# Kernel optimization log

Measured on AMD Instinct MI355X. Metric: run time of the kernel, lower is better.

The kernel has to match this reference:

```python
import jax, jax.numpy as jnp
import numpy as np
from jax import lax

BOX_STRIDES = (32, 64, 128, 256)
MASK_STRIDE = 4
MASK_SIZE = 28
PATCH = 512
TOPK = 64
SCORE_TH = 0.5
IOU_TH = 0.5
MASK_TH = 0.5


def setup_inputs():
    key = jax.random.key(0)
    ks = jax.random.split(key, 10)
    d = {}
    d["pred0"] = jax.random.normal(ks[0], (2, 6, 16, 16), jnp.float32)
    d["pred1"] = jax.random.normal(ks[1], (2, 6, 8, 8), jnp.float32)
    d["pred2"] = jax.random.normal(ks[2], (2, 6, 4, 4), jnp.float32)
    d["pred3"] = jax.random.normal(ks[3], (2, 6, 2, 2), jnp.float32)
    d["feat0"] = jax.random.normal(ks[4], (2, 64, 128, 128), jnp.float32)
    d["feat1"] = jax.random.normal(ks[5], (2, 64, 64, 64), jnp.float32)
    d["feat2"] = jax.random.normal(ks[6], (2, 64, 32, 32), jnp.float32)
    d["feat3"] = jax.random.normal(ks[7], (2, 64, 16, 16), jnp.float32)
    d["w1"] = jax.random.normal(ks[8], (128, 256, 3, 3), jnp.float32) * 0.05
    d["b1"] = jnp.zeros((128,), jnp.float32)
    d["w2"] = jax.random.normal(ks[9], (1, 128, 1, 1), jnp.float32) * 0.05
    d["b2"] = jnp.zeros((1,), jnp.float32)
    return d


def _decode_level(pred, stride):
    # pred: [B, 6, H, W] -> [B, H*W, 6], (cx,cy)=(p+grid)*stride, wh=exp(p)*stride
    B, no, H, W = pred.shape
    p = pred.transpose(0, 2, 3, 1).reshape(B, H * W, no)
    gy, gx = jnp.meshgrid(jnp.arange(H), jnp.arange(W), indexing="ij")
    grid = jnp.stack([gx.ravel(), gy.ravel()], axis=-1).astype(p.dtype)  # [HW,2] (x,y)
    xy = (p[..., 0:2] + grid) * stride
    wh = jnp.exp(p[..., 2:4]) * stride
    return jnp.concatenate([xy, wh, p[..., 4:]], axis=-1)


def _iou_matrix(b):
    # b: [K,4] xyxy
    area = jnp.clip(b[:, 2] - b[:, 0], 0) * jnp.clip(b[:, 3] - b[:, 1], 0)
    ix0 = jnp.maximum(b[:, None, 0], b[None, :, 0])
    iy0 = jnp.maximum(b[:, None, 1], b[None, :, 1])
    ix1 = jnp.minimum(b[:, None, 2], b[None, :, 2])
    iy1 = jnp.minimum(b[:, None, 3], b[None, :, 3])
    inter = jnp.clip(ix1 - ix0, 0) * jnp.clip(iy1 - iy0, 0)
    union = area[:, None] + area[None, :] - inter
    return inter / jnp.maximum(union, 1e-9)


def _nms_keep(boxes, labels, valid):
    # boxes already sorted by descending score; batched NMS via per-class coord offset
    off = labels.astype(boxes.dtype)[:, None] * (PATCH * 8.0)
    iou = _iou_matrix(boxes + off)
    idx = jnp.arange(TOPK)

    def body(i, keep):
        sup = keep[i] & (iou[i] > IOU_TH) & (idx > i)
        return keep & ~sup

    return lax.fori_loop(0, TOPK, body, valid)


def _roi_align_one(feat, box):
    # feat: [C,Hf,Wf]; box: [4] xyxy in image coords (spatial_scale=1/MASK_STRIDE)
    # torchvision-style aligned=False, one bilinear sample per bin center
    C, Hf, Wf = feat.shape
    b = box / MASK_STRIDE
    bw = (b[2] - b[0]) / MASK_SIZE
    bh = (b[3] - b[1]) / MASK_SIZE
    xs = b[0] + (jnp.arange(MASK_SIZE, dtype=feat.dtype) + 0.5) * bw
    ys = b[1] + (jnp.arange(MASK_SIZE, dtype=feat.dtype) + 0.5) * bh
    x = jnp.clip(jnp.broadcast_to(xs[None, :], (MASK_SIZE, MASK_SIZE)), 0.0, Wf - 1.0)
    y = jnp.clip(jnp.broadcast_to(ys[:, None], (MASK_SIZE, MASK_SIZE)), 0.0, Hf - 1.0)
    x0 = jnp.floor(x).astype(jnp.int32)
    y0 = jnp.floor(y).astype(jnp.int32)
    x1 = jnp.minimum(x0 + 1, Wf - 1)
    y1 = jnp.minimum(y0 + 1, Hf - 1)
    fx = x - x0
    fy = y - y0
    v00 = feat[:, y0, x0]
    v01 = feat[:, y0, x1]
    v10 = feat[:, y1, x0]
    v11 = feat[:, y1, x1]
    return (v00 * (1 - fy) * (1 - fx) + v01 * (1 - fy) * fx
            + v10 * fy * (1 - fx) + v11 * fy * fx)  # [C,S,S]


def _paste_one(mask_soft, box_int):
    # nearest-neighbor upsample of [S,S] mask into its box on a [P,P] canvas
    x0, y0, x1, y1 = box_int[0], box_int[1], box_int[2], box_int[3]
    h = y1 - y0 + 1
    w = x1 - x0 + 1
    ys = jnp.arange(PATCH, dtype=jnp.int32)
    xs = jnp.arange(PATCH, dtype=jnp.int32)
    iy = jnp.clip((ys - y0) * MASK_SIZE // h, 0, MASK_SIZE - 1)
    ix = jnp.clip((xs - x0) * MASK_SIZE // w, 0, MASK_SIZE - 1)
    g = mask_soft[iy][:, ix]  # [P,P]
    inside = ((ys >= y0) & (ys <= y1))[:, None] & ((xs >= x0) & (xs <= x1))[None, :]
    return jnp.where(inside, g, 0.0)


def _conv(x, w, b, pad):
    y = lax.conv_general_dilated(x, w, (1, 1), pad, dimension_numbers=("NCHW", "OIHW", "NCHW"))
    return y + b[None, :, None, None]


def _pipeline(pred0, pred1, pred2, pred3, feat0, feat1, feat2, feat3, w1, b1, w2, b2):
    # box branch: decode per-level predictions
    yolo = jnp.concatenate(
        [_decode_level(p, s) for p, s in zip([pred0, pred1, pred2, pred3], BOX_STRIDES)],
        axis=1,
    )  # [B,N,6]
    B = yolo.shape[0]
    cx, cy, w_, h_ = yolo[..., 0], yolo[..., 1], yolo[..., 2], yolo[..., 3]
    boxes = jnp.stack([cx - w_ / 2, cy - h_ / 2, cx + w_ / 2, cy + h_ / 2], axis=-1)
    scores = jax.nn.sigmoid(yolo[..., 4])
    labels = jnp.argmax(yolo[..., 5:], axis=-1)
    valid = scores > SCORE_TH
    top_scores, top_idx = lax.top_k(jnp.where(valid, scores, 0.0), TOPK)
    boxes_k = jnp.take_along_axis(boxes, top_idx[..., None], axis=1)  # [B,K,4]
    labels_k = jnp.take_along_axis(labels, top_idx, axis=1)
    valid_k = top_scores > SCORE_TH
    keep = jax.vmap(_nms_keep)(boxes_k, labels_k, valid_k)  # [B,K] bool

    # mask branch: merge mask feats at the first level's resolution (nearest)
    H0, W0 = feat0.shape[2], feat0.shape[3]
    merged = jnp.concatenate(
        [feat0] + [jax.image.resize(f, (B, f.shape[1], H0, W0), "nearest") for f in [feat1, feat2, feat3]],
        axis=1,
    )  # [B,256,H0,W0]
    rois = jax.vmap(lambda f, bx: jax.vmap(lambda bb: _roi_align_one(f, bb))(bx))(merged, boxes_k)
    C = rois.shape[2]
    x = rois.reshape(B * TOPK, C, MASK_SIZE, MASK_SIZE)
    hdn = jax.nn.silu(_conv(x, w1, b1, "SAME"))
    logits = _conv(hdn, w2, b2, "SAME")  # [B*K,1,S,S]
    soft = jax.nn.sigmoid(logits).reshape(B, TOPK, MASK_SIZE, MASK_SIZE)

    box_int = jnp.clip(boxes_k, 0, PATCH - 1).astype(jnp.int32)
    pasted = jax.vmap(jax.vmap(_paste_one))(soft, box_int)  # [B,K,P,P]
    return top_scores, boxes_k, labels_k, pasted, keep


def reference(pred0, pred1, pred2, pred3, feat0, feat1, feat2, feat3, w1, b1, w2, b2):
    top_scores, boxes_k, labels_k, pasted, keep = _pipeline(
        pred0, pred1, pred2, pred3, feat0, feat1, feat2, feat3, w1, b1, w2, b2
    )
    out_scores = top_scores * keep
    bin_masks = (pasted > MASK_TH) & keep[:, :, None, None]
    return out_scores, boxes_k, labels_k.astype(jnp.int32), bin_masks, keep
```

## Files before the change

### kernel.cpp

```cpp
#include <hip/hip_runtime.h>
#include <hip/hip_bf16.h>
#include <cstdint>

#define NTOPK 64
#define A_TOT 340
#define MS 28

#define OFF_SCORES 0
#define OFF_BOXES  128
#define OFF_LABELS 640
#define OFF_MASKS  768
#define OFF_KEEP   33555200ull

typedef __attribute__((ext_vector_type(4))) float f32x4;
typedef __attribute__((ext_vector_type(2))) float f32x2;
typedef long fp8x8;

__device__ __forceinline__ float sigmoidf_(float x) { return 1.f / (1.f + expf(-x)); }
__device__ __forceinline__ float bf2f(unsigned u) {
  return __uint_as_float(u << 16);
}
__device__ __forceinline__ unsigned short f2bf(float f) {
  __hip_bfloat16 h = __float2bfloat16(f);
  return *(unsigned short*)&h;
}

__global__ __launch_bounds__(256) void k_prep(
    const float* __restrict__ p0, const float* __restrict__ p1,
    const float* __restrict__ p2, const float* __restrict__ p3,
    const float* __restrict__ f0, const float* __restrict__ f1,
    const float* __restrict__ f2, const float* __restrict__ f3,
    const float* __restrict__ w1,
    float* __restrict__ out,
    float* __restrict__ ws_boxes, int* __restrict__ ws_keep,
    int* __restrict__ ws_boxint,
    unsigned char* __restrict__ wt, unsigned short* __restrict__ mg)
{
  __shared__ __align__(16) char smem_raw[128 * 260 * 2];
  const int bid = blockIdx.x;
  const int t = threadIdx.x;

  if (bid < 2) {
    const int b = bid;
    float* sc = (float*)smem_raw;
    float(*bx)[4] = (float(*)[4])(sc + A_TOT);
    float* tk_score = (float*)(bx + A_TOT);
    float(*tk_box)[4] = (float(*)[4])(tk_score + 64);

    for (int a = t; a < A_TOT; a += 256) {
      const float* pp; int W, HW, la; float stride;
      if (a < 256)      { pp = p0; W = 16; HW = 256; la = a;       stride = 32.f;  }
      else if (a < 320) { pp = p1; W = 8;  HW = 64;  la = a - 256; stride = 64.f;  }
      else if (a < 336) { pp = p2; W = 4;  HW = 16;  la = a - 320; stride = 128.f; }
      else              { pp = p3; W = 2;  HW = 4;   la = a - 336; stride = 256.f; }
      const float* base = pp + (size_t)b * 6 * HW + la;
      float v0 = base[0], v1 = base[HW], v2 = base[2 * HW], v3 = base[3 * HW], v4 = base[4 * HW];
      int gx = la % W, gy = la / W;
      float cx = (v0 + (float)gx) * stride;
      float cy = (v1 + (float)gy) * stride;
      float w_ = expf(v2) * stride;
      float h_ = expf(v3) * stride;
      float score = sigmoidf_(v4);
      sc[a] = (score > 0.5f) ? score : 0.f;
      bx[a][0] = cx - 0.5f * w_;
      bx[a][1] = cy - 0.5f * h_;
      bx[a][2] = cx + 0.5f * w_;
      bx[a][3] = cy + 0.5f * h_;
    }
    __syncthreads();

    for (int a = t; a < A_TOT; a += 256) {
      float my = sc[a];
      int rank = 0;
      for (int j = 0; j < A_TOT; ++j) {
        float o = sc[j];
        rank += (o > my) || (o == my && j < a);
      }
      if (rank < NTOPK) {
        tk_score[rank] = my;
        tk_box[rank][0] = bx[a][0];
        tk_box[rank][1] = bx[a][1];
        tk_box[rank][2] = bx[a][2];
        tk_box[rank][3] = bx[a][3];
      }
    }
    __syncthreads();

    if (t < NTOPK) {
      float x0 = tk_box[t][0], y0 = tk_box[t][1];
      float x1 = tk_box[t][2], y1 = tk_box[t][3];
      float s = tk_score[t];
      float area = fmaxf(x1 - x0, 0.f) * fmaxf(y1 - y0, 0.f);
      int keep = (s > 0.5f) ? 1 : 0;
      for (int i = 0; i < NTOPK - 1; ++i) {
        int   ki = __shfl(keep, i);
        float a0 = __shfl(x0, i);
        float c0 = __shfl(y0, i);
        float a1 = __shfl(x1, i);
        float c1 = __shfl(y1, i);
        float ai = __shfl(area, i);
        if (ki && t > i && keep) {
          float ix0 = fmaxf(a0, x0), iy0 = fmaxf(c0, y0);
          float ix1 = fminf(a1, x1), iy1 = fminf(c1, y1);
          float inter = fmaxf(ix1 - ix0, 0.f) * fmaxf(iy1 - iy0, 0.f);
          float uni = ai + area - inter;
          float iou = inter / fmaxf(uni, 1e-9f);
          if (iou > 0.5f) keep = 0;
        }
      }
      int box = b * NTOPK + t;
      out[OFF_SCORES + box] = keep ? s : 0.f;
      float bv[4] = {x0, y0, x1, y1};
      #pragma unroll
      for (int c = 0; c < 4; ++c) {
        out[OFF_BOXES + box * 4 + c] = bv[c];
        ws_boxes[box * 4 + c] = bv[c];
        float bc = fminf(fmaxf(bv[c], 0.f), 511.f);
        ws_boxint[box * 4 + c] = (int)bc;
      }
      out[OFF_LABELS + box] = 0.f;
      out[OFF_KEEP + box] = keep ? 1.f : 0.f;
      ws_keep[box] = keep;
    }
    return;
  }

  if (bid < 130) {
    const int co = bid - 2;
    const int ci = t;
    const int c = ci >> 5, cil = ci & 31;
    const int cq = co >> 5, col = co & 31;
    const int slot = ((cil >> 3) ^ ((col >> 2) & 3)) * 8 + (cil & 7);
    const float* src = w1 + ((size_t)co * 256 + ci) * 9;
    #pragma unroll
    for (int tap = 0; tap < 9; ++tap) {
      unsigned u = __builtin_amdgcn_cvt_pk_fp8_f32(src[tap], 0.f, 0, false);
      wt[(((size_t)(c * 4 + cq) * 9 + tap)) * 1024 + col * 32 + slot] =
          (unsigned char)(u & 0xff);
    }
    return;
  }

  {
    const int idx = bid - 130;
    const int b = idx >> 7;
    const int y = idx & 127;
    unsigned short* tile = (unsigned short*)smem_raw;
    const int x = t & 127, ch = t >> 7;

    {
      const float* src = f0 + ((size_t)b * 64) * 16384 + y * 128 + x;
      for (int cc = 0; cc < 32; ++cc) {
        int cl = ch * 32 + cc;
        tile[x * 260 + cl] = f2bf(src[(size_t)cl * 16384]);
      }
    }
    {
      const float* src = f1 + ((size_t)b * 64) * 4096 + (y >> 1) * 64 + (x >> 1);
      for (int cc = 0; cc < 32; ++cc) {
        int cl = ch * 32 + cc;
        tile[x * 260 + 64 + cl] = f2bf(src[(size_t)cl * 4096]);
      }
    }
    {
      const float* src = f2 + ((size_t)b * 64) * 1024 + (y >> 2) * 32 + (x >> 2);
      for (int cc = 0; cc < 32; ++cc) {
        int cl = ch * 32 + cc;
        tile[x * 260 + 128 + cl] = f2bf(src[(size_t)cl * 1024]);
      }
    }
    {
      const float* src = f3 + ((size_t)b * 64) * 256 + (y >> 3) * 16 + (x >> 3);
      for (int cc = 0; cc < 32; ++cc) {
        int cl = ch * 32 + cc;
        tile[x * 260 + 192 + cl] = f2bf(src[(size_t)cl * 256]);
      }
    }
    __syncthreads();
    unsigned short* dst = mg + (((size_t)b * 128 + y) * 128) * 256;
    for (int it = 0; it < 32; ++it) {
      int qq = t + it * 256;
      int xx = qq >> 6, cg = qq & 63;
      *(ushort4*)(dst + xx * 256 + cg * 4) = *(ushort4*)&tile[xx * 260 + cg * 4];
    }
  }
}

__global__ __launch_bounds__(512, 4) void k_conv(
    const unsigned short* __restrict__ mg,
    const unsigned char* __restrict__ wt,
    const float* __restrict__ b1, const float* __restrict__ w2,
    const float* __restrict__ b2,
    const float* __restrict__ ws_boxes, const int* __restrict__ ws_keep,
    const int* __restrict__ ws_boxint,
    float* __restrict__ out)
{
  const int bid = blockIdx.x;
  const int boxLo = bid & 7;
  const int r1 = bid >> 3;
  const int q = r1 & 3;
  const int box = ((r1 >> 2) << 3) | boxLo;
  const int t = threadIdx.x;

  float* mb = out + OFF_MASKS + (size_t)box * 262144;

  if (!ws_keep[box]) {
    f32x4 z = {0.f, 0.f, 0.f, 0.f};
    f32x4* p = (f32x4*)(mb + (size_t)q * 128 * 512);
    for (int e = t; e < 16384; e += 512)
      __builtin_nontemporal_store(z, p + e);
    return;
  }

  const int lane = t & 63, wv = t >> 6;
  const int cq = wv >> 1, half = wv & 1;
  const int laneN = lane & 15, kg = lane >> 4;

  __shared__ __align__(16) unsigned char lds[46080];
  __shared__ float psum[4][200];
  __shared__ float softm[7][28];
  __shared__ int   xa_s[MS], xb_s[MS];
  __shared__ float fx_s[MS];
  __shared__ int   ya_s[9], yb_s[9];
  __shared__ float fy_s[9];
  __shared__ float byf[4];
  __shared__ int   bii[4];

  if (t < 4) { byf[t] = ws_boxes[box * 4 + t]; bii[t] = ws_boxint[box * 4 + t]; }
  __syncthreads();
  {
    const float b0 = byf[0] * 0.25f, b1_ = byf[1] * 0.25f;
    const float b2_ = byf[2] * 0.25f, b3_ = byf[3] * 0.25f;
    if (t < MS) {
      float bw = (b2_ - b0) * (1.f / MS);
      float x = b0 + ((float)t + 0.5f) * bw;
      x = fminf(fmaxf(x, 0.f), 127.f);
      int x0 = (int)floorf(x);
      xa_s[t] = x0; xb_s[t] = min(x0 + 1, 127); fx_s[t] = x - (float)x0;
    }
    if (t < 9) {
      int gr = q * 7 + t - 1;
      if (gr < 0 || gr > 27) {
        ya_s[t] = -1; yb_s[t] = 0; fy_s[t] = 0.f;
      } else {
        float bh = (b3_ - b1_) * (1.f / MS);
        float yy = b1_ + ((float)gr + 0.5f) * bh;
        yy = fminf(fmaxf(yy, 0.f), 127.f);
        int ya = (int)floorf(yy);
        ya_s[t] = ya; yb_s[t] = min(ya + 1, 127); fy_s[t] = yy - (float)ya;
      }
    }
  }

  int badd[7][3];
  bool act[7];
  #pragma unroll
  for (int i = 0; i < 7; ++i) {
    int tile = half * 7 + i;
    act[i] = tile < 13;
    int p = tile * 16 + laneN;
    if (p > 195) p = 195;
    int py = p / 28, px = p - py * 28;
    #pragma unroll
    for (int dx = 0; dx < 3; ++dx) {
      int cell = px + dx;
      badd[i][dx] = 36864 + py * 1024 + cell * 32 + (kg ^ ((cell >> 2) & 3)) * 8;
    }
  }
  const int aswz = (kg ^ ((laneN >> 2) & 3)) * 8;

  f32x4 acc[2][7];
  #pragma unroll
  for (int m = 0; m < 2; ++m)
    #pragma unroll
    for (int i = 0; i < 7; ++i) acc[m][i] = (f32x4){0.f, 0.f, 0.f, 0.f};

  const uint4* wbase = (const uint4*)wt;
  const unsigned short* mgb = mg + ((size_t)(box >> 6) * 128 * 128) * 256;

  uint4 ga0, ga1, ga2, ga3, ga4;
  auto issueA = [&](int c) {
    const uint4* wa = wbase + (size_t)c * 2304;
    ga0 = wa[t]; ga1 = wa[t + 512]; ga2 = wa[t + 1024]; ga3 = wa[t + 1536];
    if (t < 256) ga4 = wa[t + 2048];
  };
  auto writeA = [&]() {
    uint4* da = (uint4*)lds;
    da[t] = ga0; da[t + 512] = ga1; da[t + 1024] = ga2; da[t + 1536] = ga3;
    if (t < 256) da[t + 2048] = ga4;
  };

  issueA(0);
  const unsigned char* la = lds + (size_t)cq * 9216;
  __syncthreads();

  #pragma unroll 1
  for (int c = 0; c < 8; ++c) {
    writeA();
    #pragma unroll 1
    for (int e = t; e < 1152; e += 512) {
      int r = e >> 7, rem = e & 127;
      int cell = rem >> 2, quad = rem & 3;
      unsigned char* dst = lds + 36864 + r * 1024 + cell * 32 +
                           (quad ^ ((cell >> 2) & 3)) * 8;
      int gc = cell - 1;
      int ya = ya_s[r];
      if (gc < 0 || gc > 27 || ya < 0) {
        uint2 z = {0u, 0u};
        *(uint2*)dst = z;
        continue;
      }
      int yb = yb_s[r];
      float fy = fy_s[r];
      int U = c * 4 + quad;
      int xa = xa_s[gc], xb = xb_s[gc];
      float fx = fx_s[gc];
      float w00 = (1.f - fy) * (1.f - fx), w01 = (1.f - fy) * fx;
      float w10 = fy * (1.f - fx),         w11 = fy * fx;
      uint4 A = *(const uint4*)(mgb + ((size_t)(ya * 128 + xa)) * 256 + U * 8);
      uint4 B = *(const uint4*)(mgb + ((size_t)(ya * 128 + xb)) * 256 + U * 8);
      uint4 C = *(const uint4*)(mgb + ((size_t)(yb * 128 + xa)) * 256 + U * 8);
      uint4 D = *(const uint4*)(mgb + ((size_t)(yb * 128 + xb)) * 256 + U * 8);
      const unsigned* pa = (const unsigned*)&A;
      const unsigned* pb = (const unsigned*)&B;
      const unsigned* pc = (const unsigned*)&C;
      const unsigned* pd = (const unsigned*)&D;
      float f[8];
      #pragma unroll
      for (int k2 = 0; k2 < 4; ++k2) {
        f[2 * k2] = bf2f(pa[k2] & 0xffffu) * w00 + bf2f(pb[k2] & 0xffffu) * w01 +
                    bf2f(pc[k2] & 0xffffu) * w10 + bf2f(pd[k2] & 0xffffu) * w11;
        f[2 * k2 + 1] = bf2f(pa[k2] >> 16) * w00 + bf2f(pb[k2] >> 16) * w01 +
                        bf2f(pc[k2] >> 16) * w10 + bf2f(pd[k2] >> 16) * w11;
      }
      unsigned o0 = __builtin_amdgcn_cvt_pk_fp8_f32(f[0], f[1], 0, false);
      o0 = __builtin_amdgcn_cvt_pk_fp8_f32(f[2], f[3], o0, true);
      unsigned o1 = __builtin_amdgcn_cvt_pk_fp8_f32(f[4], f[5], 0, false);
      o1 = __builtin_amdgcn_cvt_pk_fp8_f32(f[6], f[7], o1, true);
      uint2 pk; pk.x = o0; pk.y = o1;
      *(uint2*)dst = pk;
    }
    __syncthreads();
    if (c < 7) issueA(c + 1);
    #pragma unroll
    for (int tap = 0; tap < 9; ++tap) {
      const int dy = tap / 3, dx = tap - dy * 3;
      fp8x8 av0 = *(const fp8x8*)(la + tap * 1024 + laneN * 32 + aswz);
      fp8x8 av1 = *(const fp8x8*)(la + tap * 1024 + 512 + laneN * 32 + aswz);
      #pragma unroll
      for (int i = 0; i < 7; ++i) {
        if (act[i]) {
          fp8x8 bv = *(const fp8x8*)(lds + badd[i][dx] + dy * 1024);
          acc[0][i] = __builtin_amdgcn_mfma_f32_16x16x32_fp8_fp8(av0, bv, acc[0][i], 0, 0, 0);
          acc[1][i] = __builtin_amdgcn_mfma_f32_16x16x32_fp8_fp8(av1, bv, acc[1][i], 0, 0, 0);
        }
      }
    }
    __syncthreads();
  }

  {
    float b1v[2][4], w2v[2][4];
    #pragma unroll
    for (int m = 0; m < 2; ++m)
      #pragma unroll
      for (int r = 0; r < 4; ++r) {
        int co = cq * 32 + m * 16 + kg * 4 + r;
        b1v[m][r] = b1[co];
        w2v[m][r] = w2[co];
      }
    #pragma unroll
    for (int i = 0; i < 7; ++i) {
      if (!act[i]) continue;
      float part = 0.f;
      #pragma unroll
      for (int m = 0; m < 2; ++m)
        #pragma unroll
        for (int r = 0; r < 4; ++r) {
          float h = acc[m][i][r] + b1v[m][r];
          part = fmaf(w2v[m][r], h * sigmoidf_(h), part);
        }
      part += __shfl_xor(part, 16);
      part += __shfl_xor(part, 32);
      int p = (half * 7 + i) * 16 + laneN;
      if (kg == 0 && p < 196)
        psum[cq][p] = part;
    }
  }
  __syncthreads();

  if (t < 196) {
    float s = sigmoidf_(psum[0][t] + psum[1][t] + psum[2][t] + psum[3][t] + b2[0]);
    softm[t / 28][t % 28] = s;
  }
  __syncthreads();

  {
    const int x0 = bii[0], y0 = bii[1], x1 = bii[2], y1 = bii[3];
    const int w = x1 - x0 + 1, h = y1 - y0 + 1;
    int Ylo = (q == 0) ? 0 : (y0 + (q * 7 * h + 27) / 28);
    int Yhi = (q == 3) ? 512 : (y0 + ((q + 1) * 7 * h + 27) / 28);
    Ylo = min(max(Ylo, 0), 512);
    Yhi = min(max(Yhi, Ylo), 512);

    const int c4 = (t & 255) * 2;
    const int rr = t >> 8;
    int ixr[2];
    bool inx[2];
    #pragma unroll
    for (int u = 0; u < 2; ++u) {
      int X = c4 + u;
      int vx = (X - x0) * MS;
      int ix = (vx >= 0) ? (vx / w) : 0;
      ixr[u] = min(max(ix, 0), MS - 1);
      inx[u] = (X >= x0) && (X <= x1);
    }

    #pragma unroll 1
    for (int Y = Ylo + rr; Y < Yhi; Y += 2) {
      f32x2 o = {0.f, 0.f};
      if (Y >= y0 && Y <= y1) {
        int vy = (Y - y0) * MS;
        int iy = min(vy / h, MS - 1);
        const float* srow = &softm[iy - q * 7][0];
        o.x = (inx[0] && srow[ixr[0]] > 0.5f) ? 1.f : 0.f;
        o.y = (inx[1] && srow[ixr[1]] > 0.5f) ? 1.f : 0.f;
      }
      __builtin_nontemporal_store(o, (f32x2*)(mb + (size_t)Y * 512 + c4));
    }
  }
}

extern "C" void kernel_launch(void* const* d_in, const int* in_sizes, int n_in,
                              void* d_out, int out_size, void* d_ws, size_t ws_size,
                              hipStream_t stream) {
  const float* p0 = (const float*)d_in[0];
  const float* p1 = (const float*)d_in[1];
  const float* p2 = (const float*)d_in[2];
  const float* p3 = (const float*)d_in[3];
  const float* f0 = (const float*)d_in[4];
  const float* f1 = (const float*)d_in[5];
  const float* f2 = (const float*)d_in[6];
  const float* f3 = (const float*)d_in[7];
  const float* w1 = (const float*)d_in[8];
  const float* b1 = (const float*)d_in[9];
  const float* w2 = (const float*)d_in[10];
  const float* b2 = (const float*)d_in[11];
  float* out = (float*)d_out;

  float* wsf = (float*)d_ws;
  float*          ws_boxes  = wsf;
  int*            ws_keep   = (int*)(wsf + 512);
  int*            ws_boxint = (int*)(wsf + 640);
  unsigned char*  ws_wt     = (unsigned char*)(wsf + 402560);
  unsigned short* ws_merged = (unsigned short*)(wsf + 476288);

  k_prep<<<386, 256, 0, stream>>>(p0, p1, p2, p3, f0, f1, f2, f3, w1,
                                  out, ws_boxes, ws_keep, ws_boxint,
                                  ws_wt, ws_merged);
  k_conv<<<512, 512, 0, stream>>>(ws_merged, ws_wt, b1, w2, b2,
                                  ws_boxes, ws_keep, ws_boxint, out);
}
```

Before: 256.2 us.

## Software-pipeline ROI gather with MFMA and vectorize mask paste stores

The bilinear ROI gather for the next channel chunk now starts its global loads (weights and the first feature element) before the current chunk's MFMA taps, so memory latency overlaps compute. The fp8 conversion and LDS write run after the compute barrier, with an extra barrier per iteration. The mask paste now writes 16-byte float4 stores, four rows per pass, and restricts the box-row loop to rows inside the box. Rows outside the box are zero-filled in a separate loop spread across the four quarter-blocks. This adds register pressure and an extra sync per chunk.

```diff
diff --git a/kernel.cpp b/kernel.cpp
--- a/kernel.cpp
+++ b/kernel.cpp
@@ -13,7 +13,6 @@
 #define OFF_KEEP   33555200ull
 
 typedef __attribute__((ext_vector_type(4))) float f32x4;
-typedef __attribute__((ext_vector_type(2))) float f32x2;
 typedef long fp8x8;
 
 __device__ __forceinline__ float sigmoidf_(float x) { return 1.f / (1.f + expf(-x)); }
@@ -290,58 +289,75 @@
     if (t < 256) da[t + 2048] = ga4;
   };
 
+  auto loadI = [&](int i, int cn, uint4& A, uint4& B, uint4& C, uint4& D) -> bool {
+    int e = t + i * 512;
+    int r = e >> 7, rem = e & 127;
+    int cell = rem >> 2, quad = rem & 3;
+    int gc = cell - 1;
+    int ya = ya_s[r];
+    if (gc < 0 || gc > 27 || ya < 0) return true;
+    int yb = yb_s[r];
+    int xa = xa_s[gc], xb = xb_s[gc];
+    const unsigned short* bU = mgb + (size_t)(cn * 4 + quad) * 8;
+    A = *(const uint4*)(bU + (size_t)(ya * 128 + xa) * 256);
+    B = *(const uint4*)(bU + (size_t)(ya * 128 + xb) * 256);
+    C = *(const uint4*)(bU + (size_t)(yb * 128 + xa) * 256);
+    D = *(const uint4*)(bU + (size_t)(yb * 128 + xb) * 256);
+    return false;
+  };
+  auto cvtW = [&](int i, bool sk, uint4 A, uint4 B, uint4 C, uint4 D) {
+    int e = t + i * 512;
+    int r = e >> 7, rem = e & 127;
+    int cell = rem >> 2, quad = rem & 3;
+    int gc = cell - 1;
+    unsigned char* dst = lds + 36864 + r * 1024 + cell * 32 +
+                         ((quad ^ ((cell >> 2) & 3)) << 3);
+    if (sk) { uint2 z = {0u, 0u}; *(uint2*)dst = z; return; }
+    float fy = fy_s[r], fx = fx_s[gc];
+    float w00 = (1.f - fy) * (1.f - fx), w01 = (1.f - fy) * fx;
+    float w10 = fy * (1.f - fx),         w11 = fy * fx;
+    const unsigned* pa = (const unsigned*)&A;
+    const unsigned* pb = (const unsigned*)&B;
+    const unsigned* pc = (const unsigned*)&C;
+    const unsigned* pd = (const unsigned*)&D;
+    float f[8];
+    #pragma unroll
+    for (int k2 = 0; k2 < 4; ++k2) {
+      f[2 * k2] = bf2f(pa[k2] & 0xffffu) * w00 + bf2f(pb[k2] & 0xffffu) * w01 +
+                  bf2f(pc[k2] & 0xffffu) * w10 + bf2f(pd[k2] & 0xffffu) * w11;
+      f[2 * k2 + 1] = bf2f(pa[k2] >> 16) * w00 + bf2f(pb[k2] >> 16) * w01 +
+                      bf2f(pc[k2] >> 16) * w10 + bf2f(pd[k2] >> 16) * w11;
+    }
+    unsigned o0 = __builtin_amdgcn_cvt_pk_fp8_f32(f[0], f[1], 0, false);
+    o0 = __builtin_amdgcn_cvt_pk_fp8_f32(f[2], f[3], o0, true);
+    unsigned o1 = __builtin_amdgcn_cvt_pk_fp8_f32(f[4], f[5], 0, false);
+    o1 = __builtin_amdgcn_cvt_pk_fp8_f32(f[6], f[7], o1, true);
+    uint2 pk; pk.x = o0; pk.y = o1;
+    *(uint2*)dst = pk;
+  };
+
   issueA(0);
+  writeA();
+  {
+    uint4 A, B, C, D;
+    bool s0 = loadI(0, 0, A, B, C, D); cvtW(0, s0, A, B, C, D);
+    bool s1 = loadI(1, 0, A, B, C, D); cvtW(1, s1, A, B, C, D);
+    if (t < 128) {
+      bool s2 = loadI(2, 0, A, B, C, D); cvtW(2, s2, A, B, C, D);
+    }
+  }
   const unsigned char* la = lds + (size_t)cq * 9216;
   __syncthreads();
 
   #pragma unroll 1
   for (int c = 0; c < 8; ++c) {
-    writeA();
-    #pragma unroll 1
-    for (int e = t; e < 1152; e += 512) {
-      int r = e >> 7, rem = e & 127;
-      int cell = rem >> 2, quad = rem & 3;
-      unsigned char* dst = lds + 36864 + r * 1024 + cell * 32 +
-                           (quad ^ ((cell >> 2) & 3)) * 8;
-      int gc = cell - 1;
-      int ya = ya_s[r];
-      if (gc < 0 || gc > 27 || ya < 0) {
-        uint2 z = {0u, 0u};
-        *(uint2*)dst = z;
-        continue;
-      }
-      int yb = yb_s[r];
-      float fy = fy_s[r];
-      int U = c * 4 + quad;
-      int xa = xa_s[gc], xb = xb_s[gc];
-      float fx = fx_s[gc];
-      float w00 = (1.f - fy) * (1.f - fx), w01 = (1.f - fy) * fx;
-      float w10 = fy * (1.f - fx),         w11 = fy * fx;
-      uint4 A = *(const uint4*)(mgb + ((size_t)(ya * 128 + xa)) * 256 + U * 8);
-      uint4 B = *(const uint4*)(mgb + ((size_t)(ya * 128 + xb)) * 256 + U * 8);
-      uint4 C = *(const uint4*)(mgb + ((size_t)(yb * 128 + xa)) * 256 + U * 8);
-      uint4 D = *(const uint4*)(mgb + ((size_t)(yb * 128 + xb)) * 256 + U * 8);
-      const unsigned* pa = (const unsigned*)&A;
-      const unsigned* pb = (const unsigned*)&B;
-      const unsigned* pc = (const unsigned*)&C;
-      const unsigned* pd = (const unsigned*)&D;
-      float f[8];
-      #pragma unroll
-      for (int k2 = 0; k2 < 4; ++k2) {
-        f[2 * k2] = bf2f(pa[k2] & 0xffffu) * w00 + bf2f(pb[k2] & 0xffffu) * w01 +
-                    bf2f(pc[k2] & 0xffffu) * w10 + bf2f(pd[k2] & 0xffffu) * w11;
-        f[2 * k2 + 1] = bf2f(pa[k2] >> 16) * w00 + bf2f(pb[k2] >> 16) * w01 +
-                        bf2f(pc[k2] >> 16) * w10 + bf2f(pd[k2] >> 16) * w11;
-      }
-      unsigned o0 = __builtin_amdgcn_cvt_pk_fp8_f32(f[0], f[1], 0, false);
-      o0 = __builtin_amdgcn_cvt_pk_fp8_f32(f[2], f[3], o0, true);
-      unsigned o1 = __builtin_amdgcn_cvt_pk_fp8_f32(f[4], f[5], 0, false);
-      o1 = __builtin_amdgcn_cvt_pk_fp8_f32(f[6], f[7], o1, true);
-      uint2 pk; pk.x = o0; pk.y = o1;
-      *(uint2*)dst = pk;
-    }
-    __syncthreads();
-    if (c < 7) issueA(c + 1);
+    const bool pf = (c < 7);
+    uint4 A0, B0, C0, D0;
+    bool s0 = true;
+    if (pf) {
+      issueA(c + 1);
+      s0 = loadI(0, c + 1, A0, B0, C0, D0);
+    }
     #pragma unroll
     for (int tap = 0; tap < 9; ++tap) {
       const int dy = tap / 3, dx = tap - dy * 3;
@@ -357,6 +373,21 @@
       }
     }
     __syncthreads();
+    if (pf) {
+      writeA();
+      cvtW(0, s0, A0, B0, C0, D0);
+      {
+        uint4 A1, B1, C1, D1;
+        bool s1 = loadI(1, c + 1, A1, B1, C1, D1);
+        cvtW(1, s1, A1, B1, C1, D1);
+      }
+      if (t < 128) {
+        uint4 A2, B2, C2, D2;
+        bool s2 = loadI(2, c + 1, A2, B2, C2, D2);
+        cvtW(2, s2, A2, B2, C2, D2);
+      }
+      __syncthreads();
+    }
   }
 
   {
@@ -398,35 +429,41 @@
   {
     const int x0 = bii[0], y0 = bii[1], x1 = bii[2], y1 = bii[3];
     const int w = x1 - x0 + 1, h = y1 - y0 + 1;
-    int Ylo = (q == 0) ? 0 : (y0 + (q * 7 * h + 27) / 28);
-    int Yhi = (q == 3) ? 512 : (y0 + ((q + 1) * 7 * h + 27) / 28);
-    Ylo = min(max(Ylo, 0), 512);
-    Yhi = min(max(Yhi, Ylo), 512);
-
-    const int c4 = (t & 255) * 2;
-    const int rr = t >> 8;
-    int ixr[2];
-    bool inx[2];
-    #pragma unroll
-    for (int u = 0; u < 2; ++u) {
-      int X = c4 + u;
+
+    const int cg = (t & 127) * 4;
+    const int ro = t >> 7;
+    int ixr[4];
+    bool inx[4];
+    #pragma unroll
+    for (int u = 0; u < 4; ++u) {
+      int X = cg + u;
       int vx = (X - x0) * MS;
       int ix = (vx >= 0) ? (vx / w) : 0;
       ixr[u] = min(max(ix, 0), MS - 1);
       inx[u] = (X >= x0) && (X <= x1);
     }
 
+    int Ylo = y0 + (q * 7 * h + 27) / 28;
+    int Yhi = (q == 3) ? (y1 + 1) : (y0 + ((q + 1) * 7 * h + 27) / 28);
+    if (Yhi > y1 + 1) Yhi = y1 + 1;
     #pragma unroll 1
-    for (int Y = Ylo + rr; Y < Yhi; Y += 2) {
-      f32x2 o = {0.f, 0.f};
-      if (Y >= y0 && Y <= y1) {
-        int vy = (Y - y0) * MS;
-        int iy = min(vy / h, MS - 1);
-        const float* srow = &softm[iy - q * 7][0];
-        o.x = (inx[0] && srow[ixr[0]] > 0.5f) ? 1.f : 0.f;
-        o.y = (inx[1] && srow[ixr[1]] > 0.5f) ? 1.f : 0.f;
-      }
-      __builtin_nontemporal_store(o, (f32x2*)(mb + (size_t)Y * 512 + c4));
+    for (int Y = Ylo + ro; Y < Yhi; Y += 4) {
+      int vy = (Y - y0) * MS;
+      int iy = min(vy / h, MS - 1);
+      const float* srow = &softm[iy - q * 7][0];
+      f32x4 o;
+      #pragma unroll
+      for (int u = 0; u < 4; ++u)
+        o[u] = (inx[u] && srow[ixr[u]] > 0.5f) ? 1.f : 0.f;
+      __builtin_nontemporal_store(o, (f32x4*)(mb + (size_t)Y * 512 + cg));
+    }
+
+    f32x4 z = {0.f, 0.f, 0.f, 0.f};
+    #pragma unroll 1
+    for (int g = q; g < 128; g += 4) {
+      int Y = g * 4 + ro;
+      if (Y < y0 || Y > y1)
+        __builtin_nontemporal_store(z, (f32x4*)(mb + (size_t)Y * 512 + cg));
     }
   }
 }
```

New measurement: 338.7 us. +32.2%, slower.

## Compact kept boxes into dense blocks and spread zero-fill across remaining blocks

Applied to the files above, without the earlier changes.

Each conv block now builds a compacted list of kept and dropped boxes with wave ballots. The first 4*nk blocks run the conv and paste for kept boxes, and the rest share the zero-fill of dropped boxes. This replaces the fixed box-to-block mapping that left whole blocks doing only cheap zeroing. The paste stage now writes 4-wide vectors only over the box's row range and zero-fills rows outside the box in an interleaved pass. It also zeroes padding cells only on the first channel chunk and uses packed float2 math for the bilinear sampling. Every block reads all 128 keep flags, which adds a small prologue cost.

```diff
diff --git a/kernel.cpp b/kernel.cpp
--- a/kernel.cpp
+++ b/kernel.cpp
@@ -19,6 +19,12 @@
 __device__ __forceinline__ float sigmoidf_(float x) { return 1.f / (1.f + expf(-x)); }
 __device__ __forceinline__ float bf2f(unsigned u) {
   return __uint_as_float(u << 16);
+}
+__device__ __forceinline__ f32x2 up2(unsigned u) {
+  f32x2 r;
+  r.x = __uint_as_float(u << 16);
+  r.y = __uint_as_float(u & 0xffff0000u);
+  return r;
 }
 __device__ __forceinline__ unsigned short f2bf(float f) {
   __hip_bfloat16 h = __float2bfloat16(f);
@@ -196,25 +202,8 @@
     float* __restrict__ out)
 {
   const int bid = blockIdx.x;
-  const int boxLo = bid & 7;
-  const int r1 = bid >> 3;
-  const int q = r1 & 3;
-  const int box = ((r1 >> 2) << 3) | boxLo;
   const int t = threadIdx.x;
-
-  float* mb = out + OFF_MASKS + (size_t)box * 262144;
-
-  if (!ws_keep[box]) {
-    f32x4 z = {0.f, 0.f, 0.f, 0.f};
-    f32x4* p = (f32x4*)(mb + (size_t)q * 128 * 512);
-    for (int e = t; e < 16384; e += 512)
-      __builtin_nontemporal_store(z, p + e);
-    return;
-  }
-
   const int lane = t & 63, wv = t >> 6;
-  const int cq = wv >> 1, half = wv & 1;
-  const int laneN = lane & 15, kg = lane >> 4;
 
   __shared__ __align__(16) unsigned char lds[46080];
   __shared__ float psum[4][200];
@@ -225,6 +214,48 @@
   __shared__ float fy_s[9];
   __shared__ float byf[4];
   __shared__ int   bii[4];
+  __shared__ int   klist[128];
+  __shared__ int   dlist[128];
+  __shared__ int   nk_s;
+
+  if (wv == 0) {
+    int keep_l = ws_keep[lane] != 0;
+    int keep_h = ws_keep[64 + lane] != 0;
+    unsigned long long m0 = __ballot(keep_l);
+    unsigned long long m1 = __ballot(keep_h);
+    unsigned long long below = (lane == 0) ? 0ull : (~0ull >> (64 - lane));
+    int p0 = __popcll(m0);
+    if (keep_l)  klist[__popcll(m0 & below)] = lane;
+    if (keep_h)  klist[p0 + __popcll(m1 & below)] = 64 + lane;
+    if (!keep_l) dlist[__popcll(~m0 & below)] = lane;
+    if (!keep_h) dlist[(64 - p0) + __popcll(~m1 & below)] = 64 + lane;
+    if (lane == 0) nk_s = p0 + __popcll(m1);
+  }
+  __syncthreads();
+  const int nk = nk_s;
+
+  if (bid >= 4 * nk) {
+    const int L = bid - 4 * nk;
+    const int nL = 512 - 4 * nk;
+    const int nq = 4 * (128 - nk);
+    f32x4 z = {0.f, 0.f, 0.f, 0.f};
+    #pragma unroll 1
+    for (int j = L; j < nq; j += nL) {
+      float* zb = out + OFF_MASKS + (size_t)dlist[j >> 2] * 262144 +
+                  (size_t)(j & 3) * 65536;
+      f32x4* p = (f32x4*)zb;
+      for (int e = t; e < 16384; e += 512)
+        __builtin_nontemporal_store(z, p + e);
+    }
+    return;
+  }
+
+  const int box = klist[bid >> 2];
+  const int q = bid & 3;
+  float* mb = out + OFF_MASKS + (size_t)box * 262144;
+
+  const int cq = wv >> 1, half = wv & 1;
+  const int laneN = lane & 15, kg = lane >> 4;
 
   if (t < 4) { byf[t] = ws_boxes[box * 4 + t]; bii[t] = ws_boxint[box * 4 + t]; }
   __syncthreads();
@@ -302,43 +333,43 @@
       int r = e >> 7, rem = e & 127;
       int cell = rem >> 2, quad = rem & 3;
       unsigned char* dst = lds + 36864 + r * 1024 + cell * 32 +
-                           (quad ^ ((cell >> 2) & 3)) * 8;
+                           ((quad ^ ((cell >> 2) & 3)) << 3);
       int gc = cell - 1;
       int ya = ya_s[r];
       if (gc < 0 || gc > 27 || ya < 0) {
-        uint2 z = {0u, 0u};
-        *(uint2*)dst = z;
+        if (c == 0) { uint2 zz = {0u, 0u}; *(uint2*)dst = zz; }
         continue;
       }
       int yb = yb_s[r];
       float fy = fy_s[r];
-      int U = c * 4 + quad;
       int xa = xa_s[gc], xb = xb_s[gc];
       float fx = fx_s[gc];
       float w00 = (1.f - fy) * (1.f - fx), w01 = (1.f - fy) * fx;
       float w10 = fy * (1.f - fx),         w11 = fy * fx;
-      uint4 A = *(const uint4*)(mgb + ((size_t)(ya * 128 + xa)) * 256 + U * 8);
-      uint4 B = *(const uint4*)(mgb + ((size_t)(ya * 128 + xb)) * 256 + U * 8);
-      uint4 C = *(const uint4*)(mgb + ((size_t)(yb * 128 + xa)) * 256 + U * 8);
-      uint4 D = *(const uint4*)(mgb + ((size_t)(yb * 128 + xb)) * 256 + U * 8);
+      const unsigned short* bU = mgb + (size_t)(c * 4 + quad) * 8;
+      uint4 A = *(const uint4*)(bU + (size_t)(ya * 128 + xa) * 256);
+      uint4 B = *(const uint4*)(bU + (size_t)(ya * 128 + xb) * 256);
+      uint4 C = *(const uint4*)(bU + (size_t)(yb * 128 + xa) * 256);
+      uint4 D = *(const uint4*)(bU + (size_t)(yb * 128 + xb) * 256);
       const unsigned* pa = (const unsigned*)&A;
       const unsigned* pb = (const unsigned*)&B;
       const unsigned* pc = (const unsigned*)&C;
       const unsigned* pd = (const unsigned*)&D;
-      float f[8];
+      f32x2 vv[4];
       #pragma unroll
       for (int k2 = 0; k2 < 4; ++k2) {
-        f[2 * k2] = bf2f(pa[k2] & 0xffffu) * w00 + bf2f(pb[k2] & 0xffffu) * w01 +
-                    bf2f(pc[k2] & 0xffffu) * w10 + bf2f(pd[k2] & 0xffffu) * w11;
-        f[2 * k2 + 1] = bf2f(pa[k2] >> 16) * w00 + bf2f(pb[k2] >> 16) * w01 +
-                        bf2f(pc[k2] >> 16) * w10 + bf2f(pd[k2] >> 16) * w11;
-      }
-      unsigned o0 = __builtin_amdgcn_cvt_pk_fp8_f32(f[0], f[1], 0, false);
-      o0 = __builtin_amdgcn_cvt_pk_fp8_f32(f[2], f[3], o0, true);
-      unsigned o1 = __builtin_amdgcn_cvt_pk_fp8_f32(f[4], f[5], 0, false);
-      o1 = __builtin_amdgcn_cvt_pk_fp8_f32(f[6], f[7], o1, true);
-      uint2 pk; pk.x = o0; pk.y = o1;
-      *(uint2*)dst = pk;
+        f32x2 v = up2(pa[k2]) * w00;
+        v += up2(pb[k2]) * w01;
+        v += up2(pc[k2]) * w10;
+        v += up2(pd[k2]) * w11;
+        vv[k2] = v;
+      }
+      unsigned o0 = __builtin_amdgcn_cvt_pk_fp8_f32(vv[0].x, vv[0].y, 0, false);
+      o0 = __builtin_amdgcn_cvt_pk_fp8_f32(vv[1].x, vv[1].y, o0, true);
+      unsigned o1 = __builtin_amdgcn_cvt_pk_fp8_f32(vv[2].x, vv[2].y, 0, false);
+      o1 = __builtin_amdgcn_cvt_pk_fp8_f32(vv[3].x, vv[3].y, o1, true);
+      uint2 pk2; pk2.x = o0; pk2.y = o1;
+      *(uint2*)dst = pk2;
     }
     __syncthreads();
     if (c < 7) issueA(c + 1);
@@ -398,35 +429,41 @@
   {
     const int x0 = bii[0], y0 = bii[1], x1 = bii[2], y1 = bii[3];
     const int w = x1 - x0 + 1, h = y1 - y0 + 1;
-    int Ylo = (q == 0) ? 0 : (y0 + (q * 7 * h + 27) / 28);
-    int Yhi = (q == 3) ? 512 : (y0 + ((q + 1) * 7 * h + 27) / 28);
-    Ylo = min(max(Ylo, 0), 512);
-    Yhi = min(max(Yhi, Ylo), 512);
-
-    const int c4 = (t & 255) * 2;
-    const int rr = t >> 8;
-    int ixr[2];
-    bool inx[2];
-    #pragma unroll
-    for (int u = 0; u < 2; ++u) {
-      int X = c4 + u;
+
+    const int cg = (t & 127) * 4;
+    const int ro = t >> 7;
+    int ixr[4];
+    bool inx[4];
+    #pragma unroll
+    for (int u = 0; u < 4; ++u) {
+      int X = cg + u;
       int vx = (X - x0) * MS;
       int ix = (vx >= 0) ? (vx / w) : 0;
       ixr[u] = min(max(ix, 0), MS - 1);
       inx[u] = (X >= x0) && (X <= x1);
     }
 
+    int Ylo = y0 + (q * 7 * h + 27) / 28;
+    int Yhi = (q == 3) ? (y1 + 1) : (y0 + ((q + 1) * 7 * h + 27) / 28);
+    if (Yhi > y1 + 1) Yhi = y1 + 1;
     #pragma unroll 1
-    for (int Y = Ylo + rr; Y < Yhi; Y += 2) {
-      f32x2 o = {0.f, 0.f};
-      if (Y >= y0 && Y <= y1) {
-        int vy = (Y - y0) * MS;
-        int iy = min(vy / h, MS - 1);
-        const float* srow = &softm[iy - q * 7][0];
-        o.x = (inx[0] && srow[ixr[0]] > 0.5f) ? 1.f : 0.f;
-        o.y = (inx[1] && srow[ixr[1]] > 0.5f) ? 1.f : 0.f;
-      }
-      __builtin_nontemporal_store(o, (f32x2*)(mb + (size_t)Y * 512 + c4));
+    for (int Y = Ylo + ro; Y < Yhi; Y += 4) {
+      int vy = (Y - y0) * MS;
+      int iy = min(vy / h, MS - 1);
+      const float* srow = &softm[iy - q * 7][0];
+      f32x4 o;
+      #pragma unroll
+      for (int u = 0; u < 4; ++u)
+        o[u] = (inx[u] && srow[ixr[u]] > 0.5f) ? 1.f : 0.f;
+      __builtin_nontemporal_store(o, (f32x4*)(mb + (size_t)Y * 512 + cg));
+    }
+
+    f32x4 z = {0.f, 0.f, 0.f, 0.f};
+    #pragma unroll 1
+    for (int g = q; g < 128; g += 4) {
+      int Y = g * 4 + ro;
+      if (Y < y0 || Y > y1)
+        __builtin_nontemporal_store(z, (f32x4*)(mb + (size_t)Y * 512 + cg));
     }
   }
 }
```

After: 271.8 us. 6.1% more time.

## Zero all mask planes in prep kernel; paste only inside box rows

Applied to the files above, without the earlier changes.

Adds 512 extra blocks to the prep kernel that zero-fill every box's 512x512 mask plane, so the memset overlaps with the preprocessing work. The conv kernel then returns early for non-kept boxes and, for kept boxes, writes only the rows inside the box's vertical extent instead of the full quarter plane. This moves most of the large output write out of the conv kernel's tail. The cost is that kept boxes now get their planes written twice (zero fill, then the box rows), adding extra bandwidth for those boxes.

```diff
diff --git a/kernel.cpp b/kernel.cpp
--- a/kernel.cpp
+++ b/kernel.cpp
@@ -39,6 +39,17 @@
   __shared__ __align__(16) char smem_raw[128 * 260 * 2];
   const int bid = blockIdx.x;
   const int t = threadIdx.x;
+
+  if (bid >= 386) {
+    const int j = bid - 386;
+    float* zb = out + OFF_MASKS + (size_t)(j >> 2) * 262144 +
+                (size_t)(j & 3) * 65536;
+    f32x4 z = {0.f, 0.f, 0.f, 0.f};
+    f32x4* p = (f32x4*)zb;
+    for (int e = t; e < 16384; e += 256)
+      __builtin_nontemporal_store(z, p + e);
+    return;
+  }
 
   if (bid < 2) {
     const int b = bid;
@@ -202,15 +213,9 @@
   const int box = ((r1 >> 2) << 3) | boxLo;
   const int t = threadIdx.x;
 
+  if (!ws_keep[box]) return;
+
   float* mb = out + OFF_MASKS + (size_t)box * 262144;
-
-  if (!ws_keep[box]) {
-    f32x4 z = {0.f, 0.f, 0.f, 0.f};
-    f32x4* p = (f32x4*)(mb + (size_t)q * 128 * 512);
-    for (int e = t; e < 16384; e += 512)
-      __builtin_nontemporal_store(z, p + e);
-    return;
-  }
 
   const int lane = t & 63, wv = t >> 6;
   const int cq = wv >> 1, half = wv & 1;
@@ -302,7 +307,7 @@
       int r = e >> 7, rem = e & 127;
       int cell = rem >> 2, quad = rem & 3;
       unsigned char* dst = lds + 36864 + r * 1024 + cell * 32 +
-                           (quad ^ ((cell >> 2) & 3)) * 8;
+                           ((quad ^ ((cell >> 2) & 3)) << 3);
       int gc = cell - 1;
       int ya = ya_s[r];
       if (gc < 0 || gc > 27 || ya < 0) {
@@ -312,15 +317,15 @@
       }
       int yb = yb_s[r];
       float fy = fy_s[r];
-      int U = c * 4 + quad;
       int xa = xa_s[gc], xb = xb_s[gc];
       float fx = fx_s[gc];
       float w00 = (1.f - fy) * (1.f - fx), w01 = (1.f - fy) * fx;
       float w10 = fy * (1.f - fx),         w11 = fy * fx;
-      uint4 A = *(const uint4*)(mgb + ((size_t)(ya * 128 + xa)) * 256 + U * 8);
-      uint4 B = *(const uint4*)(mgb + ((size_t)(ya * 128 + xb)) * 256 + U * 8);
-      uint4 C = *(const uint4*)(mgb + ((size_t)(yb * 128 + xa)) * 256 + U * 8);
-      uint4 D = *(const uint4*)(mgb + ((size_t)(yb * 128 + xb)) * 256 + U * 8);
+      const unsigned short* bU = mgb + (size_t)(c * 4 + quad) * 8;
+      uint4 A = *(const uint4*)(bU + (size_t)(ya * 128 + xa) * 256);
+      uint4 B = *(const uint4*)(bU + (size_t)(ya * 128 + xb) * 256);
+      uint4 C = *(const uint4*)(bU + (size_t)(yb * 128 + xa) * 256);
+      uint4 D = *(const uint4*)(bU + (size_t)(yb * 128 + xb) * 256);
       const unsigned* pa = (const unsigned*)&A;
       const unsigned* pb = (const unsigned*)&B;
       const unsigned* pc = (const unsigned*)&C;
@@ -398,10 +403,10 @@
   {
     const int x0 = bii[0], y0 = bii[1], x1 = bii[2], y1 = bii[3];
     const int w = x1 - x0 + 1, h = y1 - y0 + 1;
-    int Ylo = (q == 0) ? 0 : (y0 + (q * 7 * h + 27) / 28);
-    int Yhi = (q == 3) ? 512 : (y0 + ((q + 1) * 7 * h + 27) / 28);
-    Ylo = min(max(Ylo, 0), 512);
-    Yhi = min(max(Yhi, Ylo), 512);
+
+    int Ylo = y0 + (q * 7 * h + 27) / 28;
+    int Yhi = (q == 3) ? (y1 + 1) : (y0 + ((q + 1) * 7 * h + 27) / 28);
+    if (Yhi > y1 + 1) Yhi = y1 + 1;
 
     const int c4 = (t & 255) * 2;
     const int rr = t >> 8;
@@ -418,14 +423,12 @@
 
     #pragma unroll 1
     for (int Y = Ylo + rr; Y < Yhi; Y += 2) {
-      f32x2 o = {0.f, 0.f};
-      if (Y >= y0 && Y <= y1) {
-        int vy = (Y - y0) * MS;
-        int iy = min(vy / h, MS - 1);
-        const float* srow = &softm[iy - q * 7][0];
-        o.x = (inx[0] && srow[ixr[0]] > 0.5f) ? 1.f : 0.f;
-        o.y = (inx[1] && srow[ixr[1]] > 0.5f) ? 1.f : 0.f;
-      }
+      int vy = (Y - y0) * MS;
+      int iy = min(vy / h, MS - 1);
+      const float* srow = &softm[iy - q * 7][0];
+      f32x2 o;
+      o.x = (inx[0] && srow[ixr[0]] > 0.5f) ? 1.f : 0.f;
+      o.y = (inx[1] && srow[ixr[1]] > 0.5f) ? 1.f : 0.f;
       __builtin_nontemporal_store(o, (f32x2*)(mb + (size_t)Y * 512 + c4));
     }
   }
@@ -455,7 +458,7 @@
   unsigned char*  ws_wt     = (unsigned char*)(wsf + 402560);
   unsigned short* ws_merged = (unsigned short*)(wsf + 476288);
 
-  k_prep<<<386, 256, 0, stream>>>(p0, p1, p2, p3, f0, f1, f2, f3, w1,
+  k_prep<<<898, 256, 0, stream>>>(p0, p1, p2, p3, f0, f1, f2, f3, w1,
                                   out, ws_boxes, ws_keep, ws_boxint,
                                   ws_wt, ws_merged);
   k_conv<<<512, 512, 0, stream>>>(ws_merged, ws_wt, b1, w2, b2,
```

New measurement: 247.3 us (median of 2 runs). -3.5%, faster.
